# Kernel tuning notes

Measured on AMD Instinct MI355X. Metric: run time of the kernel, lower is better.

The kernel has to match this reference:

```python
import jax, jax.numpy as jnp
import numpy as np

N = 50000        # nodes (== input_dim, featureless layer)
E = 400000       # edges in sparse support
HID = 200        # hidden dim hardcoded in GCN
NUM_CLASSES = 10


def setup_inputs() -> dict:
    key = jax.random.key(0)
    k1, k2, k3, k4 = jax.random.split(key, 4)
    return {
        "x": jnp.zeros((N, 1), dtype=jnp.float32),  # unused (featureless layer1)
        "support_rows": jax.random.randint(k1, (E,), 0, N, dtype=jnp.int32),
        "support_cols": jax.random.randint(k2, (E,), 0, N, dtype=jnp.int32),
        "support_vals": jax.random.uniform(k3, (E,), dtype=jnp.float32),
        "W0": jax.random.normal(k4, (N, HID), dtype=jnp.float32),
        "W2": jax.random.normal(jax.random.fold_in(key, 5), (HID, NUM_CLASSES), dtype=jnp.float32),
    }


def reference(x, support_rows, support_cols, support_vals, W0, W2):
    # Layer 1 (featureless): pre_sup = W0; out = A @ W0 via sparse edge list.
    # SpMM as gather + scale + segment-sum:
    gathered = W0[support_cols] * support_vals[:, None]          # [E, HID]
    h = jax.ops.segment_sum(gathered, support_rows, num_segments=N)  # [N, HID]
    h = jax.nn.relu(h)
    # Layer 2 (SimpleGraphConvolution, no act, no bias): h @ W2
    return h @ W2                                                # [N, NUM_CLASSES]
```

## Files before the change

### kernel.cpp

```cpp
#include <hip/hip_runtime.h>

#define N_NODES 50000
#define N_EDGES 400000
#define HID     200
#define NCLS    10
#define SLOTS   40


typedef unsigned uv4 __attribute__((ext_vector_type(4)));
typedef unsigned uv2 __attribute__((ext_vector_type(2)));

__device__ __forceinline__ unsigned bf16rn(float f) {
    unsigned u = __float_as_uint(f);
    return (u + 0x7FFFu + ((u >> 16) & 1u)) >> 16;
}
__device__ __forceinline__ unsigned bf16rnu(unsigned u) {
    return (u + 0x7FFFu + ((u >> 16) & 1u)) >> 16;
}
__device__ __forceinline__ float bl(unsigned u) { return __uint_as_float(u << 16); }
__device__ __forceinline__ float bh(unsigned u) { return __uint_as_float(u & 0xFFFF0000u); }

__global__ __launch_bounds__(256) void k_convert(const uv4* __restrict__ W04,
                                                 uv2* __restrict__ W0h2,
                                                 int4* __restrict__ cnt4) {
    int i = blockIdx.x * 256 + threadIdx.x;
    if (i < 12504) cnt4[i] = make_int4(0, 0, 0, 0);
    if (i >= (N_NODES * HID) / 4) return;
    uv4 f = W04[i];
    uv2 o;
    o.x = bf16rnu(f.x) | (bf16rnu(f.y) << 16);
    o.y = bf16rnu(f.z) | (bf16rnu(f.w) << 16);
    W0h2[i] = o;
}

__global__ void k_place(const int* __restrict__ rows, const int* __restrict__ cols,
                        const float* __restrict__ vals,
                        int* __restrict__ cnt, unsigned* __restrict__ ev) {
    int e = blockIdx.x * 256 + threadIdx.x;
    if (e >= N_EDGES) return;
    int r = rows[e];
    int pos = atomicAdd(&cnt[r], 1);
    if (pos < SLOTS)
        ev[(size_t)r * SLOTS + pos] = (bf16rn(vals[e]) << 16) | (unsigned)cols[e];
}

__global__ __launch_bounds__(256, 4) void gcn_fused(
        const int*      __restrict__ cnt,
        const unsigned* __restrict__ ev,
        const ushort*   __restrict__ W0h,
        const float*    __restrict__ W2,
        float*          __restrict__ out) {
    __shared__ float w2p[25 * 81 + 7];
    {
        int t = threadIdx.x;
        if (t < HID) {
            float* dst = &w2p[(t >> 3) * 81 + (t & 7) * 10];
            const float* src = &W2[t * NCLS];
            *reinterpret_cast<float4*>(dst)     = *reinterpret_cast<const float4*>(src);
            *reinterpret_cast<float4*>(dst + 4) = *reinterpret_cast<const float4*>(src + 4);
            *reinterpret_cast<float2*>(dst + 8) = *reinterpret_cast<const float2*>(src + 8);
        }
    }
    __syncthreads();

    const int lane = threadIdx.x & 63;
    const int hl   = lane & 31;
    const bool selB = lane >= 32;
    const int lp   = min(hl, 24);
    const int off8 = lp * 8;
    const float* __restrict__ w2l = &w2p[lp * 81];

    const int w  = (blockIdx.x * 256 + threadIdx.x) >> 6;
    const int wu = __builtin_amdgcn_readfirstlane(w);

    const int4 cc = *reinterpret_cast<const int4*>(cnt + 4 * wu);
    const int nA = min(cc.x, SLOTS), nB = min(cc.y, SLOTS);
    const int nC = min(cc.z, SLOTS), nD = min(cc.w, SLOTS);
    const int n0 = selB ? nC : nA;
    const int n1 = selB ? nD : nB;
    const int ntm = (max(max(nA, nB), max(nC, nD)) + 7) >> 3;

    const unsigned* __restrict__ evp = ev + (size_t)(4 * wu) * SLOTS;

    float hk0[8] = {0.f, 0.f, 0.f, 0.f, 0.f, 0.f, 0.f, 0.f};
    float hk1[8] = {0.f, 0.f, 0.f, 0.f, 0.f, 0.f, 0.f, 0.f};

    for (int t = 0; t < ntm; ++t) {
        const int s = t * 8;
        const uint4 a0 = *reinterpret_cast<const uint4*>(evp + s);
        const uint4 a1 = *reinterpret_cast<const uint4*>(evp + s + 4);
        const uint4 b0 = *reinterpret_cast<const uint4*>(evp + SLOTS + s);
        const uint4 b1 = *reinterpret_cast<const uint4*>(evp + SLOTS + s + 4);
        const uint4 c0 = *reinterpret_cast<const uint4*>(evp + 2 * SLOTS + s);
        const uint4 c1 = *reinterpret_cast<const uint4*>(evp + 2 * SLOTS + s + 4);
        const uint4 d0 = *reinterpret_cast<const uint4*>(evp + 3 * SLOTS + s);
        const uint4 d1 = *reinterpret_cast<const uint4*>(evp + 3 * SLOTS + s + 4);

        unsigned u0 = (s + 0 < n0) ? (selB ? c0.x : a0.x) : 0u;
        unsigned u1 = (s + 1 < n0) ? (selB ? c0.y : a0.y) : 0u;
        unsigned u2 = (s + 2 < n0) ? (selB ? c0.z : a0.z) : 0u;
        unsigned u3 = (s + 3 < n0) ? (selB ? c0.w : a0.w) : 0u;
        unsigned u4 = (s + 4 < n0) ? (selB ? c1.x : a1.x) : 0u;
        unsigned u5 = (s + 5 < n0) ? (selB ? c1.y : a1.y) : 0u;
        unsigned u6 = (s + 6 < n0) ? (selB ? c1.z : a1.z) : 0u;
        unsigned u7 = (s + 7 < n0) ? (selB ? c1.w : a1.w) : 0u;
        unsigned v0 = (s + 0 < n1) ? (selB ? d0.x : b0.x) : 0u;
        unsigned v1 = (s + 1 < n1) ? (selB ? d0.y : b0.y) : 0u;
        unsigned v2 = (s + 2 < n1) ? (selB ? d0.z : b0.z) : 0u;
        unsigned v3 = (s + 3 < n1) ? (selB ? d0.w : b0.w) : 0u;
        unsigned v4 = (s + 4 < n1) ? (selB ? d1.x : b1.x) : 0u;
        unsigned v5 = (s + 5 < n1) ? (selB ? d1.y : b1.y) : 0u;
        unsigned v6 = (s + 6 < n1) ? (selB ? d1.z : b1.z) : 0u;
        unsigned v7 = (s + 7 < n1) ? (selB ? d1.w : b1.w) : 0u;

        uint4 gA0 = *reinterpret_cast<const uint4*>(W0h + (size_t)(u0 & 0xFFFFu) * HID + off8);
        uint4 gA1 = *reinterpret_cast<const uint4*>(W0h + (size_t)(u1 & 0xFFFFu) * HID + off8);
        uint4 gA2 = *reinterpret_cast<const uint4*>(W0h + (size_t)(u2 & 0xFFFFu) * HID + off8);
        uint4 gA3 = *reinterpret_cast<const uint4*>(W0h + (size_t)(u3 & 0xFFFFu) * HID + off8);
        uint4 gA4 = *reinterpret_cast<const uint4*>(W0h + (size_t)(u4 & 0xFFFFu) * HID + off8);
        uint4 gA5 = *reinterpret_cast<const uint4*>(W0h + (size_t)(u5 & 0xFFFFu) * HID + off8);
        uint4 gA6 = *reinterpret_cast<const uint4*>(W0h + (size_t)(u6 & 0xFFFFu) * HID + off8);
        uint4 gA7 = *reinterpret_cast<const uint4*>(W0h + (size_t)(u7 & 0xFFFFu) * HID + off8);
        uint4 gB0 = *reinterpret_cast<const uint4*>(W0h + (size_t)(v0 & 0xFFFFu) * HID + off8);
        uint4 gB1 = *reinterpret_cast<const uint4*>(W0h + (size_t)(v1 & 0xFFFFu) * HID + off8);
        uint4 gB2 = *reinterpret_cast<const uint4*>(W0h + (size_t)(v2 & 0xFFFFu) * HID + off8);
        uint4 gB3 = *reinterpret_cast<const uint4*>(W0h + (size_t)(v3 & 0xFFFFu) * HID + off8);
        uint4 gB4 = *reinterpret_cast<const uint4*>(W0h + (size_t)(v4 & 0xFFFFu) * HID + off8);
        uint4 gB5 = *reinterpret_cast<const uint4*>(W0h + (size_t)(v5 & 0xFFFFu) * HID + off8);
        uint4 gB6 = *reinterpret_cast<const uint4*>(W0h + (size_t)(v6 & 0xFFFFu) * HID + off8);
        uint4 gB7 = *reinterpret_cast<const uint4*>(W0h + (size_t)(v7 & 0xFFFFu) * HID + off8);

#define FMA8(H, g, q) {                                                 \
        float vv = bh(q);                                               \
        H[0] += vv * bl((g).x);  H[1] += vv * bh((g).x);                \
        H[2] += vv * bl((g).y);  H[3] += vv * bh((g).y);                \
        H[4] += vv * bl((g).z);  H[5] += vv * bh((g).z);                \
        H[6] += vv * bl((g).w);  H[7] += vv * bh((g).w); }
        FMA8(hk0, gA0, u0); FMA8(hk0, gA1, u1); FMA8(hk0, gA2, u2); FMA8(hk0, gA3, u3);
        FMA8(hk0, gA4, u4); FMA8(hk0, gA5, u5); FMA8(hk0, gA6, u6); FMA8(hk0, gA7, u7);
        FMA8(hk1, gB0, v0); FMA8(hk1, gB1, v1); FMA8(hk1, gB2, v2); FMA8(hk1, gB3, v3);
        FMA8(hk1, gB4, v4); FMA8(hk1, gB5, v5); FMA8(hk1, gB6, v6); FMA8(hk1, gB7, v7);
#undef FMA8
    }

    float acc0[NCLS], acc1[NCLS];
#pragma unroll
    for (int c = 0; c < NCLS; ++c) { acc0[c] = 0.f; acc1[c] = 0.f; }
#pragma unroll
    for (int j = 0; j < 8; ++j) {
        float x0 = fmaxf(hk0[j], 0.f);
        float x1 = fmaxf(hk1[j], 0.f);
#pragma unroll
        for (int c = 0; c < NCLS; ++c) {
            float wv = w2l[j * 10 + c];
            acc0[c] += x0 * wv;
            acc1[c] += x1 * wv;
        }
    }
    const float gate = (hl < 25) ? 1.f : 0.f;
#pragma unroll
    for (int c = 0; c < NCLS; ++c) { acc0[c] *= gate; acc1[c] *= gate; }

#pragma unroll
    for (int c = 0; c < NCLS; ++c) {
#pragma unroll
        for (int off = 16; off >= 1; off >>= 1) {
            acc0[c] += __shfl_xor(acc0[c], off, 32);
            acc1[c] += __shfl_xor(acc1[c], off, 32);
        }
    }

    if (hl == 0) {
        float* o = out + (size_t)(4 * w + (selB ? 2 : 0)) * NCLS;
        *reinterpret_cast<float4*>(o)      = make_float4(acc0[0], acc0[1], acc0[2], acc0[3]);
        *reinterpret_cast<float4*>(o + 4)  = make_float4(acc0[4], acc0[5], acc0[6], acc0[7]);
        *reinterpret_cast<float4*>(o + 8)  = make_float4(acc0[8], acc0[9], acc1[0], acc1[1]);
        *reinterpret_cast<float4*>(o + 12) = make_float4(acc1[2], acc1[3], acc1[4], acc1[5]);
        *reinterpret_cast<float4*>(o + 16) = make_float4(acc1[6], acc1[7], acc1[8], acc1[9]);
    }
}

extern "C" void kernel_launch(void* const* d_in, const int* in_sizes, int n_in,
                              void* d_out, int out_size, void* d_ws, size_t ws_size,
                              hipStream_t stream) {
    const int*   rows = (const int*)  d_in[1];
    const int*   cols = (const int*)  d_in[2];
    const float* vals = (const float*)d_in[3];
    const float* W0   = (const float*)d_in[4];
    const float* W2   = (const float*)d_in[5];
    float*       out  = (float*)d_out;

    char* ws = (char*)d_ws;
    int*      cnt = (int*)     (ws);
    unsigned* ev  = (unsigned*)(ws + 200064);
    ushort*   W0h = (ushort*)  (ws + 8200064);

    int blocksC = ((N_NODES * HID) / 4 + 255) / 256;
    int blocksE = (N_EDGES + 255) / 256;

    k_convert<<<blocksC, 256, 0, stream>>>((const uv4*)W0, (uv2*)W0h, (int4*)cnt);
    k_place  <<<blocksE, 256, 0, stream>>>(rows, cols, vals, cnt, ev);

    gcn_fused<<<3125, 256, 0, stream>>>(cnt, ev, W0h, W2, out);
}
```

Measured before the change: 71.54 us.

## Fuse convert, place and aggregate into persistent kernel with grid barrier

```diff
diff --git a/kernel.cpp b/kernel.cpp
--- a/kernel.cpp
+++ b/kernel.cpp
@@ -6,6 +6,11 @@
 #define NCLS    10
 #define SLOTS   40
 
+#define MEGA_BLOCKS 1024
+#define NTHR   (MEGA_BLOCKS * 256)
+#define NWAVES (NTHR / 64)
+#define NGROUP 12500
+
 
 typedef unsigned uv4 __attribute__((ext_vector_type(4)));
 typedef unsigned uv2 __attribute__((ext_vector_type(2)));
@@ -20,36 +25,22 @@
 __device__ __forceinline__ float bl(unsigned u) { return __uint_as_float(u << 16); }
 __device__ __forceinline__ float bh(unsigned u) { return __uint_as_float(u & 0xFFFF0000u); }
 
-__global__ __launch_bounds__(256) void k_convert(const uv4* __restrict__ W04,
-                                                 uv2* __restrict__ W0h2,
-                                                 int4* __restrict__ cnt4) {
+__global__ __launch_bounds__(256) void k_init(int4* __restrict__ z) {
     int i = blockIdx.x * 256 + threadIdx.x;
-    if (i < 12504) cnt4[i] = make_int4(0, 0, 0, 0);
-    if (i >= (N_NODES * HID) / 4) return;
-    uv4 f = W04[i];
-    uv2 o;
-    o.x = bf16rnu(f.x) | (bf16rnu(f.y) << 16);
-    o.y = bf16rnu(f.z) | (bf16rnu(f.w) << 16);
-    W0h2[i] = o;
-}
-
-__global__ void k_place(const int* __restrict__ rows, const int* __restrict__ cols,
-                        const float* __restrict__ vals,
-                        int* __restrict__ cnt, unsigned* __restrict__ ev) {
-    int e = blockIdx.x * 256 + threadIdx.x;
-    if (e >= N_EDGES) return;
-    int r = rows[e];
-    int pos = atomicAdd(&cnt[r], 1);
-    if (pos < SLOTS)
-        ev[(size_t)r * SLOTS + pos] = (bf16rn(vals[e]) << 16) | (unsigned)cols[e];
-}
-
-__global__ __launch_bounds__(256, 4) void gcn_fused(
-        const int*      __restrict__ cnt,
-        const unsigned* __restrict__ ev,
-        const ushort*   __restrict__ W0h,
-        const float*    __restrict__ W2,
-        float*          __restrict__ out) {
+    if (i < 12508) z[i] = make_int4(0, 0, 0, 0);
+}
+
+__global__ __launch_bounds__(256, 4) void k_mega(
+        const int*   __restrict__ rows,
+        const int*   __restrict__ cols,
+        const float* __restrict__ vals,
+        const uv4*   __restrict__ W04,
+        const float* __restrict__ W2,
+        float*       __restrict__ out,
+        int*         __restrict__ cnt,
+        int*         __restrict__ bar,
+        unsigned*    __restrict__ ev,
+        ushort*      __restrict__ W0h) {
     __shared__ float w2p[25 * 81 + 7];
     {
         int t = threadIdx.x;
@@ -61,6 +52,43 @@
             *reinterpret_cast<float2*>(dst + 8) = *reinterpret_cast<const float2*>(src + 8);
         }
     }
+
+    const int tid = blockIdx.x * 256 + threadIdx.x;
+
+    for (int e = tid; e < N_EDGES; e += NTHR) {
+        int r = rows[e];
+        int pos = atomicAdd(&cnt[r], 1);
+        if (pos < SLOTS)
+            ev[(size_t)r * SLOTS + pos] = (bf16rn(vals[e]) << 16) | (unsigned)cols[e];
+    }
+
+    {
+        uv2* __restrict__ W0h2 = reinterpret_cast<uv2*>(W0h);
+        const int NQ = (N_NODES * HID) / 4;
+        for (int i = tid; i < NQ; i += NTHR) {
+            uv4 f = W04[i];
+            uv2 o;
+            o.x = bf16rnu(f.x) | (bf16rnu(f.y) << 16);
+            o.y = bf16rnu(f.z) | (bf16rnu(f.w) << 16);
+            W0h2[i] = o;
+        }
+    }
+
+    __syncthreads();
+    if (threadIdx.x == 0) {
+        __threadfence();
+        int prev = __hip_atomic_fetch_add(&bar[0], 1, __ATOMIC_ACQ_REL,
+                                          __HIP_MEMORY_SCOPE_AGENT);
+        if (prev == MEGA_BLOCKS - 1) {
+            __hip_atomic_store(&bar[1], 1, __ATOMIC_RELEASE,
+                               __HIP_MEMORY_SCOPE_AGENT);
+        } else {
+            while (__hip_atomic_load(&bar[1], __ATOMIC_ACQUIRE,
+                                     __HIP_MEMORY_SCOPE_AGENT) == 0)
+                __builtin_amdgcn_s_sleep(2);
+        }
+        __threadfence();
+    }
     __syncthreads();
 
     const int lane = threadIdx.x & 63;
@@ -69,114 +97,123 @@
     const int lp   = min(hl, 24);
     const int off8 = lp * 8;
     const float* __restrict__ w2l = &w2p[lp * 81];
-
-    const int w  = (blockIdx.x * 256 + threadIdx.x) >> 6;
-    const int wu = __builtin_amdgcn_readfirstlane(w);
-
-    const int4 cc = *reinterpret_cast<const int4*>(cnt + 4 * wu);
-    const int nA = min(cc.x, SLOTS), nB = min(cc.y, SLOTS);
-    const int nC = min(cc.z, SLOTS), nD = min(cc.w, SLOTS);
-    const int n0 = selB ? nC : nA;
-    const int n1 = selB ? nD : nB;
-    const int ntm = (max(max(nA, nB), max(nC, nD)) + 7) >> 3;
-
-    const unsigned* __restrict__ evp = ev + (size_t)(4 * wu) * SLOTS;
-
-    float hk0[8] = {0.f, 0.f, 0.f, 0.f, 0.f, 0.f, 0.f, 0.f};
-    float hk1[8] = {0.f, 0.f, 0.f, 0.f, 0.f, 0.f, 0.f, 0.f};
-
-    for (int t = 0; t < ntm; ++t) {
-        const int s = t * 8;
-        const uint4 a0 = *reinterpret_cast<const uint4*>(evp + s);
-        const uint4 a1 = *reinterpret_cast<const uint4*>(evp + s + 4);
-        const uint4 b0 = *reinterpret_cast<const uint4*>(evp + SLOTS + s);
-        const uint4 b1 = *reinterpret_cast<const uint4*>(evp + SLOTS + s + 4);
-        const uint4 c0 = *reinterpret_cast<const uint4*>(evp + 2 * SLOTS + s);
-        const uint4 c1 = *reinterpret_cast<const uint4*>(evp + 2 * SLOTS + s + 4);
-        const uint4 d0 = *reinterpret_cast<const uint4*>(evp + 3 * SLOTS + s);
-        const uint4 d1 = *reinterpret_cast<const uint4*>(evp + 3 * SLOTS + s + 4);
-
-        unsigned u0 = (s + 0 < n0) ? (selB ? c0.x : a0.x) : 0u;
-        unsigned u1 = (s + 1 < n0) ? (selB ? c0.y : a0.y) : 0u;
-        unsigned u2 = (s + 2 < n0) ? (selB ? c0.z : a0.z) : 0u;
-        unsigned u3 = (s + 3 < n0) ? (selB ? c0.w : a0.w) : 0u;
-        unsigned u4 = (s + 4 < n0) ? (selB ? c1.x : a1.x) : 0u;
-        unsigned u5 = (s + 5 < n0) ? (selB ? c1.y : a1.y) : 0u;
-        unsigned u6 = (s + 6 < n0) ? (selB ? c1.z : a1.z) : 0u;
-        unsigned u7 = (s + 7 < n0) ? (selB ? c1.w : a1.w) : 0u;
-        unsigned v0 = (s + 0 < n1) ? (selB ? d0.x : b0.x) : 0u;
-        unsigned v1 = (s + 1 < n1) ? (selB ? d0.y : b0.y) : 0u;
-        unsigned v2 = (s + 2 < n1) ? (selB ? d0.z : b0.z) : 0u;
-        unsigned v3 = (s + 3 < n1) ? (selB ? d0.w : b0.w) : 0u;
-        unsigned v4 = (s + 4 < n1) ? (selB ? d1.x : b1.x) : 0u;
-        unsigned v5 = (s + 5 < n1) ? (selB ? d1.y : b1.y) : 0u;
-        unsigned v6 = (s + 6 < n1) ? (selB ? d1.z : b1.z) : 0u;
-        unsigned v7 = (s + 7 < n1) ? (selB ? d1.w : b1.w) : 0u;
-
-        uint4 gA0 = *reinterpret_cast<const uint4*>(W0h + (size_t)(u0 & 0xFFFFu) * HID + off8);
-        uint4 gA1 = *reinterpret_cast<const uint4*>(W0h + (size_t)(u1 & 0xFFFFu) * HID + off8);
-        uint4 gA2 = *reinterpret_cast<const uint4*>(W0h + (size_t)(u2 & 0xFFFFu) * HID + off8);
-        uint4 gA3 = *reinterpret_cast<const uint4*>(W0h + (size_t)(u3 & 0xFFFFu) * HID + off8);
-        uint4 gA4 = *reinterpret_cast<const uint4*>(W0h + (size_t)(u4 & 0xFFFFu) * HID + off8);
-        uint4 gA5 = *reinterpret_cast<const uint4*>(W0h + (size_t)(u5 & 0xFFFFu) * HID + off8);
-        uint4 gA6 = *reinterpret_cast<const uint4*>(W0h + (size_t)(u6 & 0xFFFFu) * HID + off8);
-        uint4 gA7 = *reinterpret_cast<const uint4*>(W0h + (size_t)(u7 & 0xFFFFu) * HID + off8);
-        uint4 gB0 = *reinterpret_cast<const uint4*>(W0h + (size_t)(v0 & 0xFFFFu) * HID + off8);
-        uint4 gB1 = *reinterpret_cast<const uint4*>(W0h + (size_t)(v1 & 0xFFFFu) * HID + off8);
-        uint4 gB2 = *reinterpret_cast<const uint4*>(W0h + (size_t)(v2 & 0xFFFFu) * HID + off8);
-        uint4 gB3 = *reinterpret_cast<const uint4*>(W0h + (size_t)(v3 & 0xFFFFu) * HID + off8);
-        uint4 gB4 = *reinterpret_cast<const uint4*>(W0h + (size_t)(v4 & 0xFFFFu) * HID + off8);
-        uint4 gB5 = *reinterpret_cast<const uint4*>(W0h + (size_t)(v5 & 0xFFFFu) * HID + off8);
-        uint4 gB6 = *reinterpret_cast<const uint4*>(W0h + (size_t)(v6 & 0xFFFFu) * HID + off8);
-        uint4 gB7 = *reinterpret_cast<const uint4*>(W0h + (size_t)(v7 & 0xFFFFu) * HID + off8);
+    const int wid = tid >> 6;
+
+    for (int g0 = wid; g0 < NGROUP; g0 += NWAVES) {
+        const int g = __builtin_amdgcn_readfirstlane(g0);
+
+        unsigned long long cAB = __hip_atomic_load(
+            reinterpret_cast<const unsigned long long*>(cnt + 4 * g),
+            __ATOMIC_RELAXED, __HIP_MEMORY_SCOPE_AGENT);
+        unsigned long long cCD = __hip_atomic_load(
+            reinterpret_cast<const unsigned long long*>(cnt + 4 * g + 2),
+            __ATOMIC_RELAXED, __HIP_MEMORY_SCOPE_AGENT);
+        const int nA = min((int)(unsigned)(cAB & 0xFFFFFFFFull), SLOTS);
+        const int nB = min((int)(unsigned)(cAB >> 32), SLOTS);
+        const int nC = min((int)(unsigned)(cCD & 0xFFFFFFFFull), SLOTS);
+        const int nD = min((int)(unsigned)(cCD >> 32), SLOTS);
+        const int n0 = selB ? nC : nA;
+        const int n1 = selB ? nD : nB;
+        const int ntm = (max(max(nA, nB), max(nC, nD)) + 7) >> 3;
+
+        const unsigned* __restrict__ evp = ev + (size_t)(4 * g) * SLOTS;
+
+        float hk0[8] = {0.f, 0.f, 0.f, 0.f, 0.f, 0.f, 0.f, 0.f};
+        float hk1[8] = {0.f, 0.f, 0.f, 0.f, 0.f, 0.f, 0.f, 0.f};
+
+        for (int t = 0; t < ntm; ++t) {
+            const int s = t * 8;
+            const uint4 a0 = *reinterpret_cast<const uint4*>(evp + s);
+            const uint4 a1 = *reinterpret_cast<const uint4*>(evp + s + 4);
+            const uint4 b0 = *reinterpret_cast<const uint4*>(evp + SLOTS + s);
+            const uint4 b1 = *reinterpret_cast<const uint4*>(evp + SLOTS + s + 4);
+            const uint4 c0 = *reinterpret_cast<const uint4*>(evp + 2 * SLOTS + s);
+            const uint4 c1 = *reinterpret_cast<const uint4*>(evp + 2 * SLOTS + s + 4);
+            const uint4 d0 = *reinterpret_cast<const uint4*>(evp + 3 * SLOTS + s);
+            const uint4 d1 = *reinterpret_cast<const uint4*>(evp + 3 * SLOTS + s + 4);
+
+            unsigned u0 = (s + 0 < n0) ? (selB ? c0.x : a0.x) : 0u;
+            unsigned u1 = (s + 1 < n0) ? (selB ? c0.y : a0.y) : 0u;
+            unsigned u2 = (s + 2 < n0) ? (selB ? c0.z : a0.z) : 0u;
+            unsigned u3 = (s + 3 < n0) ? (selB ? c0.w : a0.w) : 0u;
+            unsigned u4 = (s + 4 < n0) ? (selB ? c1.x : a1.x) : 0u;
+            unsigned u5 = (s + 5 < n0) ? (selB ? c1.y : a1.y) : 0u;
+            unsigned u6 = (s + 6 < n0) ? (selB ? c1.z : a1.z) : 0u;
+            unsigned u7 = (s + 7 < n0) ? (selB ? c1.w : a1.w) : 0u;
+            unsigned v0 = (s + 0 < n1) ? (selB ? d0.x : b0.x) : 0u;
+            unsigned v1 = (s + 1 < n1) ? (selB ? d0.y : b0.y) : 0u;
+            unsigned v2 = (s + 2 < n1) ? (selB ? d0.z : b0.z) : 0u;
+            unsigned v3 = (s + 3 < n1) ? (selB ? d0.w : b0.w) : 0u;
+            unsigned v4 = (s + 4 < n1) ? (selB ? d1.x : b1.x) : 0u;
+            unsigned v5 = (s + 5 < n1) ? (selB ? d1.y : b1.y) : 0u;
+            unsigned v6 = (s + 6 < n1) ? (selB ? d1.z : b1.z) : 0u;
+            unsigned v7 = (s + 7 < n1) ? (selB ? d1.w : b1.w) : 0u;
+
+            uint4 gA0 = *reinterpret_cast<const uint4*>(W0h + (size_t)(u0 & 0xFFFFu) * HID + off8);
+            uint4 gA1 = *reinterpret_cast<const uint4*>(W0h + (size_t)(u1 & 0xFFFFu) * HID + off8);
+            uint4 gA2 = *reinterpret_cast<const uint4*>(W0h + (size_t)(u2 & 0xFFFFu) * HID + off8);
+            uint4 gA3 = *reinterpret_cast<const uint4*>(W0h + (size_t)(u3 & 0xFFFFu) * HID + off8);
+            uint4 gA4 = *reinterpret_cast<const uint4*>(W0h + (size_t)(u4 & 0xFFFFu) * HID + off8);
+            uint4 gA5 = *reinterpret_cast<const uint4*>(W0h + (size_t)(u5 & 0xFFFFu) * HID + off8);
+            uint4 gA6 = *reinterpret_cast<const uint4*>(W0h + (size_t)(u6 & 0xFFFFu) * HID + off8);
+            uint4 gA7 = *reinterpret_cast<const uint4*>(W0h + (size_t)(u7 & 0xFFFFu) * HID + off8);
+            uint4 gB0 = *reinterpret_cast<const uint4*>(W0h + (size_t)(v0 & 0xFFFFu) * HID + off8);
+            uint4 gB1 = *reinterpret_cast<const uint4*>(W0h + (size_t)(v1 & 0xFFFFu) * HID + off8);
+            uint4 gB2 = *reinterpret_cast<const uint4*>(W0h + (size_t)(v2 & 0xFFFFu) * HID + off8);
+            uint4 gB3 = *reinterpret_cast<const uint4*>(W0h + (size_t)(v3 & 0xFFFFu) * HID + off8);
+            uint4 gB4 = *reinterpret_cast<const uint4*>(W0h + (size_t)(v4 & 0xFFFFu) * HID + off8);
+            uint4 gB5 = *reinterpret_cast<const uint4*>(W0h + (size_t)(v5 & 0xFFFFu) * HID + off8);
+            uint4 gB6 = *reinterpret_cast<const uint4*>(W0h + (size_t)(v6 & 0xFFFFu) * HID + off8);
+            uint4 gB7 = *reinterpret_cast<const uint4*>(W0h + (size_t)(v7 & 0xFFFFu) * HID + off8);
 
 #define FMA8(H, g, q) {                                                 \
-        float vv = bh(q);                                               \
-        H[0] += vv * bl((g).x);  H[1] += vv * bh((g).x);                \
-        H[2] += vv * bl((g).y);  H[3] += vv * bh((g).y);                \
-        H[4] += vv * bl((g).z);  H[5] += vv * bh((g).z);                \
-        H[6] += vv * bl((g).w);  H[7] += vv * bh((g).w); }
-        FMA8(hk0, gA0, u0); FMA8(hk0, gA1, u1); FMA8(hk0, gA2, u2); FMA8(hk0, gA3, u3);
-        FMA8(hk0, gA4, u4); FMA8(hk0, gA5, u5); FMA8(hk0, gA6, u6); FMA8(hk0, gA7, u7);
-        FMA8(hk1, gB0, v0); FMA8(hk1, gB1, v1); FMA8(hk1, gB2, v2); FMA8(hk1, gB3, v3);
-        FMA8(hk1, gB4, v4); FMA8(hk1, gB5, v5); FMA8(hk1, gB6, v6); FMA8(hk1, gB7, v7);
+            float vv = bh(q);                                           \
+            H[0] += vv * bl((g).x);  H[1] += vv * bh((g).x);            \
+            H[2] += vv * bl((g).y);  H[3] += vv * bh((g).y);            \
+            H[4] += vv * bl((g).z);  H[5] += vv * bh((g).z);            \
+            H[6] += vv * bl((g).w);  H[7] += vv * bh((g).w); }
+            FMA8(hk0, gA0, u0); FMA8(hk0, gA1, u1); FMA8(hk0, gA2, u2); FMA8(hk0, gA3, u3);
+            FMA8(hk0, gA4, u4); FMA8(hk0, gA5, u5); FMA8(hk0, gA6, u6); FMA8(hk0, gA7, u7);
+            FMA8(hk1, gB0, v0); FMA8(hk1, gB1, v1); FMA8(hk1, gB2, v2); FMA8(hk1, gB3, v3);
+            FMA8(hk1, gB4, v4); FMA8(hk1, gB5, v5); FMA8(hk1, gB6, v6); FMA8(hk1, gB7, v7);
 #undef FMA8
-    }
-
-    float acc0[NCLS], acc1[NCLS];
-#pragma unroll
-    for (int c = 0; c < NCLS; ++c) { acc0[c] = 0.f; acc1[c] = 0.f; }
-#pragma unroll
-    for (int j = 0; j < 8; ++j) {
-        float x0 = fmaxf(hk0[j], 0.f);
-        float x1 = fmaxf(hk1[j], 0.f);
+        }
+
+        float acc0[NCLS], acc1[NCLS];
+#pragma unroll
+        for (int c = 0; c < NCLS; ++c) { acc0[c] = 0.f; acc1[c] = 0.f; }
+#pragma unroll
+        for (int j = 0; j < 8; ++j) {
+            float x0 = fmaxf(hk0[j], 0.f);
+            float x1 = fmaxf(hk1[j], 0.f);
+#pragma unroll
+            for (int c = 0; c < NCLS; ++c) {
+                float wv = w2l[j * 10 + c];
+                acc0[c] += x0 * wv;
+                acc1[c] += x1 * wv;
+            }
+        }
+        const float gate = (hl < 25) ? 1.f : 0.f;
+#pragma unroll
+        for (int c = 0; c < NCLS; ++c) { acc0[c] *= gate; acc1[c] *= gate; }
+
 #pragma unroll
         for (int c = 0; c < NCLS; ++c) {
-            float wv = w2l[j * 10 + c];
-            acc0[c] += x0 * wv;
-            acc1[c] += x1 * wv;
-        }
-    }
-    const float gate = (hl < 25) ? 1.f : 0.f;
-#pragma unroll
-    for (int c = 0; c < NCLS; ++c) { acc0[c] *= gate; acc1[c] *= gate; }
-
-#pragma unroll
-    for (int c = 0; c < NCLS; ++c) {
-#pragma unroll
-        for (int off = 16; off >= 1; off >>= 1) {
-            acc0[c] += __shfl_xor(acc0[c], off, 32);
-            acc1[c] += __shfl_xor(acc1[c], off, 32);
-        }
-    }
-
-    if (hl == 0) {
-        float* o = out + (size_t)(4 * w + (selB ? 2 : 0)) * NCLS;
-        *reinterpret_cast<float4*>(o)      = make_float4(acc0[0], acc0[1], acc0[2], acc0[3]);
-        *reinterpret_cast<float4*>(o + 4)  = make_float4(acc0[4], acc0[5], acc0[6], acc0[7]);
-        *reinterpret_cast<float4*>(o + 8)  = make_float4(acc0[8], acc0[9], acc1[0], acc1[1]);
-        *reinterpret_cast<float4*>(o + 12) = make_float4(acc1[2], acc1[3], acc1[4], acc1[5]);
-        *reinterpret_cast<float4*>(o + 16) = make_float4(acc1[6], acc1[7], acc1[8], acc1[9]);
+#pragma unroll
+            for (int off = 16; off >= 1; off >>= 1) {
+                acc0[c] += __shfl_xor(acc0[c], off, 32);
+                acc1[c] += __shfl_xor(acc1[c], off, 32);
+            }
+        }
+
+        if (hl == 0) {
+            float* o = out + (size_t)(4 * g0 + (selB ? 2 : 0)) * NCLS;
+            *reinterpret_cast<float4*>(o)      = make_float4(acc0[0], acc0[1], acc0[2], acc0[3]);
+            *reinterpret_cast<float4*>(o + 4)  = make_float4(acc0[4], acc0[5], acc0[6], acc0[7]);
+            *reinterpret_cast<float4*>(o + 8)  = make_float4(acc0[8], acc0[9], acc1[0], acc1[1]);
+            *reinterpret_cast<float4*>(o + 12) = make_float4(acc1[2], acc1[3], acc1[4], acc1[5]);
+            *reinterpret_cast<float4*>(o + 16) = make_float4(acc1[6], acc1[7], acc1[8], acc1[9]);
+        }
     }
 }
 
@@ -192,14 +229,12 @@
 
     char* ws = (char*)d_ws;
     int*      cnt = (int*)     (ws);
-    unsigned* ev  = (unsigned*)(ws + 200064);
-    ushort*   W0h = (ushort*)  (ws + 8200064);
-
-    int blocksC = ((N_NODES * HID) / 4 + 255) / 256;
-    int blocksE = (N_EDGES + 255) / 256;
-
-    k_convert<<<blocksC, 256, 0, stream>>>((const uv4*)W0, (uv2*)W0h, (int4*)cnt);
-    k_place  <<<blocksE, 256, 0, stream>>>(rows, cols, vals, cnt, ev);
-
-    gcn_fused<<<3125, 256, 0, stream>>>(cnt, ev, W0h, W2, out);
-}
+    int*      bar = (int*)     (ws + 200064);
+    unsigned* ev  = (unsigned*)(ws + 200128);
+    ushort*   W0h = (ushort*)  (ws + 8200128);
+
+    k_init<<<49, 256, 0, stream>>>((int4*)ws);
+
+    k_mega<<<MEGA_BLOCKS, 256, 0, stream>>>(
+        rows, cols, vals, (const uv4*)W0, W2, out, cnt, bar, ev, W0h);
+}
```

New measurement: 282.1 us. 294% more time.
